# Kernel tuning notes

Measured on AMD Instinct MI355X. Metric: run time of the kernel, lower is better.

## Reference

```python
import jax, jax.numpy as jnp
import numpy as np

DIM = 384
NUM_HEADS = 12
KERNEL = 3
DILATIONS = (1, 2, 3)
B, H, W = 16, 56, 56


def _unfold(x, k, dil):
    # x: [B, c, H, W] -> [B, c, k*k, H, W]; matches nn.Unfold(k, dilation=dil,
    # padding=dil*(k-1)//2, stride=1) channel ordering [c, kh, kw].
    b, c, h, w = x.shape
    p = dil * (k - 1) // 2
    xp = jnp.pad(x, ((0, 0), (0, 0), (p, p), (p, p)))
    patches = [xp[:, :, i * dil:i * dil + h, j * dil:j * dil + w]
               for i in range(k) for j in range(k)]
    return jnp.stack(patches, axis=2)


def _dilate_attention(q, k, v, head_dim, kernel, dil):
    # q,k,v: [B, c, H, W]
    b, c, h, w = q.shape
    g = c // head_dim           # heads in this dilation branch
    kk = kernel * kernel
    scale = head_dim ** (-0.5)
    qg = q.reshape(b, g, head_dim, h * w)                       # [b,g,d,n]
    ku = _unfold(k, kernel, dil).reshape(b, g, head_dim, kk, h * w)
    vu = _unfold(v, kernel, dil).reshape(b, g, head_dim, kk, h * w)
    attn = jnp.einsum('bgdn,bgdkn->bgnk', qg, ku) * scale       # [b,g,n,kk]
    attn = jax.nn.softmax(attn, axis=-1)
    out = jnp.einsum('bgnk,bgdkn->bgnd', attn, vu)              # [b,g,n,d]
    return out.transpose(0, 2, 1, 3).reshape(b, h, w, c)        # [b,h,w,c]


def setup_inputs() -> dict:
    key = jax.random.key(0)
    kx, kq, kp = jax.random.split(key, 3)
    x = jax.random.normal(kx, (B, H, W, DIM), dtype=jnp.float32)
    w_qkv = jax.random.normal(kq, (3 * DIM, DIM), dtype=jnp.float32) * 0.02
    w_proj = jax.random.normal(kp, (DIM, DIM), dtype=jnp.float32) * 0.02
    b_proj = jnp.zeros((DIM,), dtype=jnp.float32)
    return {"x": x, "w_qkv": w_qkv, "w_proj": w_proj, "b_proj": b_proj}


def reference(x, w_qkv, w_proj, b_proj):
    b, h, w, c = x.shape
    nd = len(DILATIONS)
    cg = c // nd                # channels per dilation branch
    hd = c // NUM_HEADS         # head_dim
    xc = x.transpose(0, 3, 1, 2)                                 # [b,c,h,w]
    qkv = jnp.einsum('bchw,oc->bohw', xc, w_qkv)                 # 1x1 conv, no bias
    qkv = qkv.reshape(b, 3, nd, cg, h, w)
    outs = [_dilate_attention(qkv[:, 0, i], qkv[:, 1, i], qkv[:, 2, i],
                              hd, KERNEL, DILATIONS[i]) for i in range(nd)]
    y = jnp.stack(outs, axis=3).reshape(b, h, w, c)              # [b,h,w, nd*cg]
    return jnp.einsum('bhwc,oc->bhwo', y, w_proj) + b_proj
```

## Files before the change

### kernel.cpp

```cpp
#include <hip/hip_runtime.h>
#include <hip/hip_bf16.h>


#define NTOK 50176
#define ROWQKV 1152
#define CDIM 384

typedef _Float16 half2v __attribute__((ext_vector_type(2)));
typedef _Float16 half8 __attribute__((ext_vector_type(8)));
typedef float floatx4 __attribute__((ext_vector_type(4)));

typedef __attribute__((address_space(1))) const unsigned int GU32;
typedef __attribute__((address_space(3))) unsigned int LU32;

#define N_X4 (NTOK * CDIM / 4)
#define N_Q4 (ROWQKV * CDIM / 4)
#define N_P4 (CDIM * CDIM / 4)

__global__ __launch_bounds__(256) void conv_all(const float* __restrict__ x,
                                                const float* __restrict__ wq,
                                                const float* __restrict__ wp,
                                                _Float16* __restrict__ xh,
                                                _Float16* __restrict__ wqh,
                                                _Float16* __restrict__ wph) {
  const int total = N_X4 + N_Q4 + N_P4;
  int i = blockIdx.x * 256 + threadIdx.x;
  const int stride = gridDim.x * 256;
  for (; i < total; i += stride) {
    const float* src;
    _Float16* dst;
    int k;
    if (i < N_X4) { src = x; dst = xh; k = i; }
    else if (i < N_X4 + N_Q4) { src = wq; dst = wqh; k = i - N_X4; }
    else { src = wp; dst = wph; k = i - N_X4 - N_Q4; }
    float4 v = ((const float4*)src)[k];
    union { _Float16 h[4]; uint2 u; } o;
    o.h[0] = (_Float16)v.x; o.h[1] = (_Float16)v.y;
    o.h[2] = (_Float16)v.z; o.h[3] = (_Float16)v.w;
    ((uint2*)dst)[k] = o.u;
  }
}

template <bool HALF_OUT>
__global__ __launch_bounds__(256) void gemm3(const _Float16* __restrict__ A,
                                             const _Float16* __restrict__ B,
                                             const float* __restrict__ bias,
                                             void* __restrict__ Cout,
                                             int N, int K) {
  __shared__ _Float16 As[2][128 * 32];
  __shared__ _Float16 Bs[2][128 * 32];
  const int tid = threadIdx.x;
  const int lane = tid & 63;
  const int wv = tid >> 6;
  const int wr = wv >> 1, wc = wv & 1;

  const int nN = N >> 7;
  const int p = blockIdx.x;
  const int l = (p & 7) * (gridDim.x >> 3) + (p >> 3);
  const size_t row0 = (size_t)(l / nN) * 128;
  const int col0 = (l % nN) * 128;
  const int NT = K / 32;

  const int srow = tid >> 2;
  const int gslot = (tid & 3) ^ ((srow >> 1) & 3);
  const _Float16* Abase = A + (row0 + srow) * (size_t)K + gslot * 8;
  const _Float16* Bbase = B + ((size_t)(col0 + srow)) * (size_t)K + gslot * 8;
  char* AsB = (char*)As;
  char* BsB = (char*)Bs;

  auto stage = [&](int k0, int buf) {
    __builtin_amdgcn_global_load_lds((GU32*)(Abase + k0),
                                     (LU32*)(AsB + buf * 8192 + tid * 16), 16, 0, 0);
    __builtin_amdgcn_global_load_lds((GU32*)(Abase + (size_t)64 * K + k0),
                                     (LU32*)(AsB + buf * 8192 + tid * 16 + 4096), 16, 0, 0);
    __builtin_amdgcn_global_load_lds((GU32*)(Bbase + k0),
                                     (LU32*)(BsB + buf * 8192 + tid * 16), 16, 0, 0);
    __builtin_amdgcn_global_load_lds((GU32*)(Bbase + (size_t)64 * K + k0),
                                     (LU32*)(BsB + buf * 8192 + tid * 16 + 4096), 16, 0, 0);
  };

  const int fr = lane & 15;
  const int fq = lane >> 4;
  const int rpos = (fq ^ ((fr >> 1) & 3)) * 8;

  floatx4 acc[4][4];
#pragma unroll
  for (int i = 0; i < 4; ++i)
#pragma unroll
    for (int j = 0; j < 4; ++j) acc[i][j] = (floatx4){0.f, 0.f, 0.f, 0.f};

  stage(0, 0);
  asm volatile("s_waitcnt vmcnt(0)" ::: "memory");
  __builtin_amdgcn_s_barrier();

  int cur = 0;
  for (int t = 0; t < NT; ++t) {
    if (t + 1 < NT) {
      stage((t + 1) * 32, cur ^ 1);
      asm volatile("s_waitcnt vmcnt(4)" ::: "memory");
    } else {
      asm volatile("s_waitcnt vmcnt(0)" ::: "memory");
    }
    __builtin_amdgcn_s_barrier();
    __builtin_amdgcn_sched_barrier(0);
    half8 af[4], bf[4];
#pragma unroll
    for (int f = 0; f < 4; ++f) {
      af[f] = *(const half8*)&As[cur][(wr * 64 + f * 16 + fr) * 32 + rpos];
      bf[f] = *(const half8*)&Bs[cur][(wc * 64 + f * 16 + fr) * 32 + rpos];
    }
#pragma unroll
    for (int i = 0; i < 4; ++i)
#pragma unroll
      for (int j = 0; j < 4; ++j)
        acc[i][j] = __builtin_amdgcn_mfma_f32_16x16x32_f16(af[i], bf[j], acc[i][j], 0, 0, 0);
    __builtin_amdgcn_sched_barrier(0);
    __builtin_amdgcn_s_barrier();
    cur ^= 1;
  }

  const int crow = wr * 64 + (lane >> 4) * 4;
  const int ccol = wc * 64 + (lane & 15);
#pragma unroll
  for (int fm = 0; fm < 4; ++fm) {
#pragma unroll
    for (int fn = 0; fn < 4; ++fn) {
      const size_t r0 = (row0 + crow + fm * 16) * (size_t)N + col0 + ccol + fn * 16;
      if (HALF_OUT) {
        _Float16* C = (_Float16*)Cout;
#pragma unroll
        for (int j = 0; j < 4; ++j) C[r0 + (size_t)j * N] = (_Float16)acc[fm][fn][j];
      } else {
        float* C = (float*)Cout;
        const float bz = bias[col0 + ccol + fn * 16];
#pragma unroll
        for (int j = 0; j < 4; ++j) C[r0 + (size_t)j * N] = acc[fm][fn][j] + bz;
      }
    }
  }
}

__global__ __launch_bounds__(256) void attn_kernel(const _Float16* __restrict__ qkv,
                                                   _Float16* __restrict__ y) {
  const int idx = blockIdx.x * 256 + threadIdx.x;
  const int head = idx % 12;
  const int token = idx / 12;
  const int branch = head >> 2;
  const int dil = branch + 1;
  const int cbase = branch * 128 + (head & 3) * 32;
  const int xx = token % 56;
  const int yy = (token / 56) % 56;
  const int bimg = token / 3136;
  const float scale = 0.17677669529663687f;

  const _Float16* qp = qkv + (size_t)token * ROWQKV + cbase;
  half2v qh[16];
  *(half8*)&qh[0] = *(const half8*)(qp);
  *(half8*)&qh[4] = *(const half8*)(qp + 8);
  *(half8*)&qh[8] = *(const half8*)(qp + 16);
  *(half8*)&qh[12] = *(const half8*)(qp + 24);

  const size_t nbase = (size_t)bimg * 3136;

  float l[9];
#pragma unroll
  for (int j = 0; j < 9; ++j) {
    const int ny = yy + (j / 3 - 1) * dil;
    const int nx = xx + (j % 3 - 1) * dil;
    float d = 0.f;
    if ((unsigned)ny < 56u && (unsigned)nx < 56u) {
      const _Float16* kp = qkv + (nbase + ny * 56 + nx) * ROWQKV + 384 + cbase;
      half2v kh[16];
      *(half8*)&kh[0] = *(const half8*)(kp);
      *(half8*)&kh[4] = *(const half8*)(kp + 8);
      *(half8*)&kh[8] = *(const half8*)(kp + 16);
      *(half8*)&kh[12] = *(const half8*)(kp + 24);
#if __has_builtin(__builtin_amdgcn_fdot2)
#pragma unroll
      for (int c = 0; c < 16; ++c) d = __builtin_amdgcn_fdot2(qh[c], kh[c], d, false);
#else
#pragma unroll
      for (int c = 0; c < 16; ++c)
        d += (float)qh[c][0] * (float)kh[c][0] + (float)qh[c][1] * (float)kh[c][1];
#endif
    }
    l[j] = d * scale;
  }

  float m = l[0];
#pragma unroll
  for (int j = 1; j < 9; ++j) m = fmaxf(m, l[j]);
  float s = 0.f;
#pragma unroll
  for (int j = 0; j < 9; ++j) { l[j] = expf(l[j] - m); s += l[j]; }
  const float rs = 1.f / s;

  float out[32];
#pragma unroll
  for (int c = 0; c < 32; ++c) out[c] = 0.f;
#pragma unroll
  for (int j = 0; j < 9; ++j) {
    const int ny = yy + (j / 3 - 1) * dil;
    const int nx = xx + (j % 3 - 1) * dil;
    if ((unsigned)ny < 56u && (unsigned)nx < 56u) {
      const _Float16* vp = qkv + (nbase + ny * 56 + nx) * ROWQKV + 768 + cbase;
      half8 vh[4];
      vh[0] = *(const half8*)(vp);
      vh[1] = *(const half8*)(vp + 8);
      vh[2] = *(const half8*)(vp + 16);
      vh[3] = *(const half8*)(vp + 24);
      const float p = l[j];
#pragma unroll
      for (int g = 0; g < 4; ++g)
#pragma unroll
        for (int e = 0; e < 8; ++e) out[g * 8 + e] = fmaf(p, (float)vh[g][e], out[g * 8 + e]);
    }
  }

  _Float16* yp = y + (size_t)token * CDIM + cbase;
  half8 oh[4];
#pragma unroll
  for (int g = 0; g < 4; ++g) {
#pragma unroll
    for (int e = 0; e < 8; ++e) oh[g][e] = (_Float16)(out[g * 8 + e] * rs);
    *(half8*)(yp + g * 8) = oh[g];
  }
}

extern "C" void kernel_launch(void* const* d_in, const int* in_sizes, int n_in,
                              void* d_out, int out_size, void* d_ws, size_t ws_size,
                              hipStream_t stream) {
  const float* x = (const float*)d_in[0];
  const float* w_qkv = (const float*)d_in[1];
  const float* w_proj = (const float*)d_in[2];
  const float* b_proj = (const float*)d_in[3];
  float* out = (float*)d_out;

  _Float16* xh = (_Float16*)d_ws;
  _Float16* wqh = xh + (size_t)NTOK * CDIM;
  _Float16* wph = wqh + (size_t)ROWQKV * CDIM;
  _Float16* qkvh = wph + (size_t)CDIM * CDIM;
  _Float16* yh = qkvh + (size_t)NTOK * ROWQKV;

  conv_all<<<2048, 256, 0, stream>>>(x, w_qkv, w_proj, xh, wqh, wph);

  gemm3<true><<<(NTOK / 128) * (ROWQKV / 128), 256, 0, stream>>>(
      xh, wqh, nullptr, qkvh, ROWQKV, CDIM);

  attn_kernel<<<(NTOK * 12) / 256, 256, 0, stream>>>(qkvh, yh);

  gemm3<false><<<(NTOK / 128) * (CDIM / 128), 256, 0, stream>>>(
      yh, wph, b_proj, out, CDIM, CDIM);
}
```

Baseline: 183.3 us.

## Replace QKV GEMM with 256x256-tile 8-wave kernel and pad N to 1280

Adds a dedicated QKV projection GEMM that uses 256x256 output tiles with 512 threads, a K-tile of 64, XOR-swizzled LDS staging, split A fragment loads and s_setprio around the MFMA bursts. The output row stride is padded from 1152 to 1280 so the N dimension divides evenly into 256-wide tiles, and the attention kernel indexing and workspace layout are updated to match. The aim is more data reuse per LDS load and fewer blocks than the 128x128 generic kernel. The cost is about 11% extra MFMA work and extra qkv write traffic for padding columns that are computed from uninitialized weight rows and never read, plus lower occupancy from one large block per CU.

```diff
diff --git a/kernel.cpp b/kernel.cpp
--- a/kernel.cpp
+++ b/kernel.cpp
@@ -4,6 +4,7 @@
 
 #define NTOK 50176
 #define ROWQKV 1152
+#define NQP 1280
 #define CDIM 384
 
 typedef _Float16 half2v __attribute__((ext_vector_type(2)));
@@ -41,14 +42,125 @@
   }
 }
 
+__global__ __launch_bounds__(512, 1) void gemm_qkv8(const _Float16* __restrict__ A,
+                                                    const _Float16* __restrict__ B,
+                                                    _Float16* __restrict__ C) {
+  __shared__ _Float16 As[2][256 * 64];
+  __shared__ _Float16 Bs[2][256 * 64];
+  const int tid = threadIdx.x;
+  const int lane = tid & 63;
+  const int wv = tid >> 6;
+  const int wr = wv >> 2;
+  const int wc = wv & 3;
+  const int K = CDIM;
+
+  const int p = blockIdx.x;
+  const int xcd = p & 7, bi = p >> 3;
+  const int q = gridDim.x >> 3, r = gridDim.x & 7;
+  const int l = (xcd < r) ? xcd * (q + 1) + bi : r * (q + 1) + (xcd - r) * q + bi;
+  const int nN = NQP / 256;
+  const size_t row0 = (size_t)(l / nN) * 256;
+  const int col0 = (l % nN) * 256;
+
+  const int sr = tid >> 3;
+  const int ss = tid & 7;
+  const int aslot = (ss ^ (sr & 7)) * 8;
+  char* AsB = (char*)As;
+  char* BsB = (char*)Bs;
+
+  auto stage = [&](int kt, int buf) {
+    const int k0 = kt * 64;
+#pragma unroll
+    for (int c = 0; c < 4; ++c)
+      __builtin_amdgcn_global_load_lds(
+          (GU32*)(A + (row0 + c * 64 + sr) * (size_t)K + k0 + aslot),
+          (LU32*)(AsB + buf * 32768 + c * 8192 + tid * 16), 16, 0, 0);
+#pragma unroll
+    for (int c = 0; c < 4; ++c)
+      __builtin_amdgcn_global_load_lds(
+          (GU32*)(B + ((size_t)(col0 + c * 64 + sr)) * K + k0 + aslot),
+          (LU32*)(BsB + buf * 32768 + c * 8192 + tid * 16), 16, 0, 0);
+  };
+
+  const int fr = lane & 15;
+  const int fq = lane >> 4;
+  const int frm = fr & 7;
+
+  floatx4 acc[8][4];
+#pragma unroll
+  for (int m = 0; m < 8; ++m)
+#pragma unroll
+    for (int n = 0; n < 4; ++n) acc[m][n] = (floatx4){0.f, 0.f, 0.f, 0.f};
+
+  stage(0, 0);
+  asm volatile("s_waitcnt vmcnt(0)" ::: "memory");
+  __builtin_amdgcn_s_barrier();
+
+  for (int kt = 0; kt < 6; ++kt) {
+    const int buf = kt & 1;
+    if (kt < 5) {
+      stage(kt + 1, buf ^ 1);
+      asm volatile("s_waitcnt vmcnt(8)" ::: "memory");
+    } else {
+      asm volatile("s_waitcnt vmcnt(0)" ::: "memory");
+    }
+    __builtin_amdgcn_s_barrier();
+    __builtin_amdgcn_sched_barrier(0);
+
+    const char* ab = AsB + buf * 32768;
+    const char* bb = BsB + buf * 32768;
+    half8 af[4], bf[4];
+#pragma unroll
+    for (int kh = 0; kh < 2; ++kh) {
+      const int ko = ((((kh << 2) | fq) ^ frm) << 4);
+#pragma unroll
+      for (int half = 0; half < 2; ++half) {
+        const int mbase = half * 4;
+        if (half == 0) {
+#pragma unroll
+          for (int n = 0; n < 4; ++n)
+            bf[n] = *(const half8*)(bb + (wc * 64 + n * 16 + fr) * 128 + ko);
+        }
+#pragma unroll
+        for (int mg = 0; mg < 4; ++mg)
+          af[mg] = *(const half8*)(ab + (wr * 128 + (mbase + mg) * 16 + fr) * 128 + ko);
+        asm volatile("s_waitcnt lgkmcnt(0)" ::: "memory");
+        __builtin_amdgcn_sched_barrier(0);
+        __builtin_amdgcn_s_setprio(1);
+#pragma unroll
+        for (int mg = 0; mg < 4; ++mg)
+#pragma unroll
+          for (int n = 0; n < 4; ++n)
+            acc[mbase + mg][n] = __builtin_amdgcn_mfma_f32_16x16x32_f16(
+                af[mg], bf[n], acc[mbase + mg][n], 0, 0, 0);
+        __builtin_amdgcn_s_setprio(0);
+        __builtin_amdgcn_sched_barrier(0);
+        __builtin_amdgcn_s_barrier();
+      }
+    }
+  }
+
+  const int crow0 = wr * 128 + (lane >> 4) * 4;
+  const int ccol0 = wc * 64 + (lane & 15);
+#pragma unroll
+  for (int m = 0; m < 8; ++m) {
+#pragma unroll
+    for (int n = 0; n < 4; ++n) {
+      const size_t r0 = (row0 + crow0 + m * 16) * (size_t)NQP + col0 + ccol0 + n * 16;
+#pragma unroll
+      for (int j = 0; j < 4; ++j) C[r0 + (size_t)j * NQP] = (_Float16)acc[m][n][j];
+    }
+  }
+}
+
 template <bool HALF_OUT>
 __global__ __launch_bounds__(256) void gemm3(const _Float16* __restrict__ A,
                                              const _Float16* __restrict__ B,
                                              const float* __restrict__ bias,
                                              void* __restrict__ Cout,
                                              int N, int K) {
-  __shared__ _Float16 As[2][128 * 32];
-  __shared__ _Float16 Bs[2][128 * 32];
+  __shared__ _Float16 Asl[2][128 * 32];
+  __shared__ _Float16 Bsl[2][128 * 32];
   const int tid = threadIdx.x;
   const int lane = tid & 63;
   const int wv = tid >> 6;
@@ -65,8 +177,8 @@
   const int gslot = (tid & 3) ^ ((srow >> 1) & 3);
   const _Float16* Abase = A + (row0 + srow) * (size_t)K + gslot * 8;
   const _Float16* Bbase = B + ((size_t)(col0 + srow)) * (size_t)K + gslot * 8;
-  char* AsB = (char*)As;
-  char* BsB = (char*)Bs;
+  char* AsB = (char*)Asl;
+  char* BsB = (char*)Bsl;
 
   auto stage = [&](int k0, int buf) {
     __builtin_amdgcn_global_load_lds((GU32*)(Abase + k0),
@@ -106,8 +218,8 @@
     half8 af[4], bf[4];
 #pragma unroll
     for (int f = 0; f < 4; ++f) {
-      af[f] = *(const half8*)&As[cur][(wr * 64 + f * 16 + fr) * 32 + rpos];
-      bf[f] = *(const half8*)&Bs[cur][(wc * 64 + f * 16 + fr) * 32 + rpos];
+      af[f] = *(const half8*)&Asl[cur][(wr * 64 + f * 16 + fr) * 32 + rpos];
+      bf[f] = *(const half8*)&Bsl[cur][(wc * 64 + f * 16 + fr) * 32 + rpos];
     }
 #pragma unroll
     for (int i = 0; i < 4; ++i)
@@ -127,14 +239,14 @@
     for (int fn = 0; fn < 4; ++fn) {
       const size_t r0 = (row0 + crow + fm * 16) * (size_t)N + col0 + ccol + fn * 16;
       if (HALF_OUT) {
-        _Float16* C = (_Float16*)Cout;
-#pragma unroll
-        for (int j = 0; j < 4; ++j) C[r0 + (size_t)j * N] = (_Float16)acc[fm][fn][j];
+        _Float16* Cc = (_Float16*)Cout;
+#pragma unroll
+        for (int j = 0; j < 4; ++j) Cc[r0 + (size_t)j * N] = (_Float16)acc[fm][fn][j];
       } else {
-        float* C = (float*)Cout;
+        float* Cc = (float*)Cout;
         const float bz = bias[col0 + ccol + fn * 16];
 #pragma unroll
-        for (int j = 0; j < 4; ++j) C[r0 + (size_t)j * N] = acc[fm][fn][j] + bz;
+        for (int j = 0; j < 4; ++j) Cc[r0 + (size_t)j * N] = acc[fm][fn][j] + bz;
       }
     }
   }
@@ -153,7 +265,7 @@
   const int bimg = token / 3136;
   const float scale = 0.17677669529663687f;
 
-  const _Float16* qp = qkv + (size_t)token * ROWQKV + cbase;
+  const _Float16* qp = qkv + (size_t)token * NQP + cbase;
   half2v qh[16];
   *(half8*)&qh[0] = *(const half8*)(qp);
   *(half8*)&qh[4] = *(const half8*)(qp + 8);
@@ -169,7 +281,7 @@
     const int nx = xx + (j % 3 - 1) * dil;
     float d = 0.f;
     if ((unsigned)ny < 56u && (unsigned)nx < 56u) {
-      const _Float16* kp = qkv + (nbase + ny * 56 + nx) * ROWQKV + 384 + cbase;
+      const _Float16* kp = qkv + (nbase + ny * 56 + nx) * NQP + 384 + cbase;
       half2v kh[16];
       *(half8*)&kh[0] = *(const half8*)(kp);
       *(half8*)&kh[4] = *(const half8*)(kp + 8);
@@ -203,7 +315,7 @@
     const int ny = yy + (j / 3 - 1) * dil;
     const int nx = xx + (j % 3 - 1) * dil;
     if ((unsigned)ny < 56u && (unsigned)nx < 56u) {
-      const _Float16* vp = qkv + (nbase + ny * 56 + nx) * ROWQKV + 768 + cbase;
+      const _Float16* vp = qkv + (nbase + ny * 56 + nx) * NQP + 768 + cbase;
       half8 vh[4];
       vh[0] = *(const half8*)(vp);
       vh[1] = *(const half8*)(vp + 8);
@@ -238,14 +350,13 @@
 
   _Float16* xh = (_Float16*)d_ws;
   _Float16* wqh = xh + (size_t)NTOK * CDIM;
-  _Float16* wph = wqh + (size_t)ROWQKV * CDIM;
+  _Float16* wph = wqh + (size_t)NQP * CDIM;
   _Float16* qkvh = wph + (size_t)CDIM * CDIM;
-  _Float16* yh = qkvh + (size_t)NTOK * ROWQKV;
+  _Float16* yh = qkvh + (size_t)NTOK * NQP;
 
   conv_all<<<2048, 256, 0, stream>>>(x, w_qkv, w_proj, xh, wqh, wph);
 
-  gemm3<true><<<(NTOK / 128) * (ROWQKV / 128), 256, 0, stream>>>(
-      xh, wqh, nullptr, qkvh, ROWQKV, CDIM);
+  gemm_qkv8<<<(NTOK / 256) * (NQP / 256), 512, 0, stream>>>(xh, wqh, qkvh);
 
   attn_kernel<<<(NTOK * 12) / 256, 256, 0, stream>>>(qkvh, yh);
 
```

New measurement: 187.2 us. 2.1% more time.

## Tile dilated attention per 8x8 patch with shared-memory K/V halo staging

Applied to the files above, without the earlier changes.

Replaces the per-thread attention kernel, which gathered nine K and V rows straight from global memory, with a templated kernel per dilation. Each kernel loads an 8x8 token tile plus its dilation halo of K/V into padded shared memory, then serves every neighbour lookup from LDS. Out-of-image neighbours are stored as zeros, so the bounds branches in the inner loops go away. The cost is three separate launches and a large LDS footprint for the biggest dilation (about 110KB), which limits occupancy to roughly one block per CU. Some GEMM variables are also renamed.

```diff
diff --git a/kernel.cpp b/kernel.cpp
--- a/kernel.cpp
+++ b/kernel.cpp
@@ -47,8 +47,8 @@
                                              const float* __restrict__ bias,
                                              void* __restrict__ Cout,
                                              int N, int K) {
-  __shared__ _Float16 As[2][128 * 32];
-  __shared__ _Float16 Bs[2][128 * 32];
+  __shared__ _Float16 Asl[2][128 * 32];
+  __shared__ _Float16 Bsl[2][128 * 32];
   const int tid = threadIdx.x;
   const int lane = tid & 63;
   const int wv = tid >> 6;
@@ -65,8 +65,8 @@
   const int gslot = (tid & 3) ^ ((srow >> 1) & 3);
   const _Float16* Abase = A + (row0 + srow) * (size_t)K + gslot * 8;
   const _Float16* Bbase = B + ((size_t)(col0 + srow)) * (size_t)K + gslot * 8;
-  char* AsB = (char*)As;
-  char* BsB = (char*)Bs;
+  char* AsB = (char*)Asl;
+  char* BsB = (char*)Bsl;
 
   auto stage = [&](int k0, int buf) {
     __builtin_amdgcn_global_load_lds((GU32*)(Abase + k0),
@@ -106,8 +106,8 @@
     half8 af[4], bf[4];
 #pragma unroll
     for (int f = 0; f < 4; ++f) {
-      af[f] = *(const half8*)&As[cur][(wr * 64 + f * 16 + fr) * 32 + rpos];
-      bf[f] = *(const half8*)&Bs[cur][(wc * 64 + f * 16 + fr) * 32 + rpos];
+      af[f] = *(const half8*)&Asl[cur][(wr * 64 + f * 16 + fr) * 32 + rpos];
+      bf[f] = *(const half8*)&Bsl[cur][(wc * 64 + f * 16 + fr) * 32 + rpos];
     }
 #pragma unroll
     for (int i = 0; i < 4; ++i)
@@ -127,63 +127,85 @@
     for (int fn = 0; fn < 4; ++fn) {
       const size_t r0 = (row0 + crow + fm * 16) * (size_t)N + col0 + ccol + fn * 16;
       if (HALF_OUT) {
-        _Float16* C = (_Float16*)Cout;
-#pragma unroll
-        for (int j = 0; j < 4; ++j) C[r0 + (size_t)j * N] = (_Float16)acc[fm][fn][j];
+        _Float16* Cc = (_Float16*)Cout;
+#pragma unroll
+        for (int j = 0; j < 4; ++j) Cc[r0 + (size_t)j * N] = (_Float16)acc[fm][fn][j];
       } else {
-        float* C = (float*)Cout;
+        float* Cc = (float*)Cout;
         const float bz = bias[col0 + ccol + fn * 16];
 #pragma unroll
-        for (int j = 0; j < 4; ++j) C[r0 + (size_t)j * N] = acc[fm][fn][j] + bz;
+        for (int j = 0; j < 4; ++j) Cc[r0 + (size_t)j * N] = acc[fm][fn][j] + bz;
       }
     }
   }
 }
 
-__global__ __launch_bounds__(256) void attn_kernel(const _Float16* __restrict__ qkv,
-                                                   _Float16* __restrict__ y) {
-  const int idx = blockIdx.x * 256 + threadIdx.x;
-  const int head = idx % 12;
-  const int token = idx / 12;
-  const int branch = head >> 2;
-  const int dil = branch + 1;
-  const int cbase = branch * 128 + (head & 3) * 32;
-  const int xx = token % 56;
-  const int yy = (token / 56) % 56;
-  const int bimg = token / 3136;
+template <int DIL>
+__global__ __launch_bounds__(256) void attn_tile(const _Float16* __restrict__ qkv,
+                                                 _Float16* __restrict__ y) {
+  constexpr int H = 8 + 2 * DIL;
+  constexpr int NROW = H * H;
+  __shared__ char kv[NROW * 560];
+  const int tid = threadIdx.x;
+  const int head = tid & 3;
+  const int tok = tid >> 2;
+  const int ly = tok >> 3, lx = tok & 7;
+  const int branch = DIL - 1;
+  const int cb = branch * 128;
+  const int bimg = blockIdx.y;
+  const int ty0 = (blockIdx.x / 7) * 8;
+  const int tx0 = (blockIdx.x % 7) * 8;
+  const size_t base = (size_t)bimg * 3136;
   const float scale = 0.17677669529663687f;
 
-  const _Float16* qp = qkv + (size_t)token * ROWQKV + cbase;
+  constexpr int NG = NROW * 32;
+  for (int g = tid; g < NG; g += 256) {
+    const int r = g >> 5, sl = g & 31;
+    const int gy = ty0 - DIL + r / H;
+    const int gx = tx0 - DIL + r % H;
+    uint4 val = make_uint4(0u, 0u, 0u, 0u);
+    if ((unsigned)gy < 56u && (unsigned)gx < 56u) {
+      const int off = (sl < 16) ? (384 + cb + sl * 8) : (768 + cb + (sl - 16) * 8);
+      val = *(const uint4*)(qkv + (base + gy * 56 + gx) * ROWQKV + off);
+    }
+    *(uint4*)(kv + r * 560 + sl * 16) = val;
+  }
+
+  const int gty = ty0 + ly, gtx = tx0 + lx;
+  const _Float16* qp = qkv + (base + gty * 56 + gtx) * ROWQKV + cb + head * 32;
   half2v qh[16];
   *(half8*)&qh[0] = *(const half8*)(qp);
   *(half8*)&qh[4] = *(const half8*)(qp + 8);
   *(half8*)&qh[8] = *(const half8*)(qp + 16);
   *(half8*)&qh[12] = *(const half8*)(qp + 24);
 
-  const size_t nbase = (size_t)bimg * 3136;
+  __syncthreads();
+
+  int rtap[9];
+#pragma unroll
+  for (int j = 0; j < 9; ++j) {
+    const int dy = j / 3 - 1, dx = j % 3 - 1;
+    rtap[j] = (ly + DIL + dy * DIL) * H + (lx + DIL + dx * DIL);
+  }
 
   float l[9];
 #pragma unroll
   for (int j = 0; j < 9; ++j) {
-    const int ny = yy + (j / 3 - 1) * dil;
-    const int nx = xx + (j % 3 - 1) * dil;
+    const char* kp = kv + rtap[j] * 560 + head * 64;
+    half2v kh[16];
+    *(half8*)&kh[0] = *(const half8*)(kp);
+    *(half8*)&kh[4] = *(const half8*)(kp + 16);
+    *(half8*)&kh[8] = *(const half8*)(kp + 32);
+    *(half8*)&kh[12] = *(const half8*)(kp + 48);
     float d = 0.f;
-    if ((unsigned)ny < 56u && (unsigned)nx < 56u) {
-      const _Float16* kp = qkv + (nbase + ny * 56 + nx) * ROWQKV + 384 + cbase;
-      half2v kh[16];
-      *(half8*)&kh[0] = *(const half8*)(kp);
-      *(half8*)&kh[4] = *(const half8*)(kp + 8);
-      *(half8*)&kh[8] = *(const half8*)(kp + 16);
-      *(half8*)&kh[12] = *(const half8*)(kp + 24);
 #if __has_builtin(__builtin_amdgcn_fdot2)
 #pragma unroll
-      for (int c = 0; c < 16; ++c) d = __builtin_amdgcn_fdot2(qh[c], kh[c], d, false);
+    for (int c = 0; c < 16; ++c) d = __builtin_amdgcn_fdot2(qh[c], kh[c], d, false);
 #else
 #pragma unroll
-      for (int c = 0; c < 16; ++c)
-        d += (float)qh[c][0] * (float)kh[c][0] + (float)qh[c][1] * (float)kh[c][1];
+    for (int c = 0; c < 16; ++c)
+      d += (float)qh[c][0] * (float)kh[c][0] + (float)qh[c][1] * (float)kh[c][1];
 #endif
-    }
     l[j] = d * scale;
   }
 
@@ -200,24 +222,20 @@
   for (int c = 0; c < 32; ++c) out[c] = 0.f;
 #pragma unroll
   for (int j = 0; j < 9; ++j) {
-    const int ny = yy + (j / 3 - 1) * dil;
-    const int nx = xx + (j % 3 - 1) * dil;
-    if ((unsigned)ny < 56u && (unsigned)nx < 56u) {
-      const _Float16* vp = qkv + (nbase + ny * 56 + nx) * ROWQKV + 768 + cbase;
-      half8 vh[4];
-      vh[0] = *(const half8*)(vp);
-      vh[1] = *(const half8*)(vp + 8);
-      vh[2] = *(const half8*)(vp + 16);
-      vh[3] = *(const half8*)(vp + 24);
-      const float p = l[j];
-#pragma unroll
-      for (int g = 0; g < 4; ++g)
-#pragma unroll
-        for (int e = 0; e < 8; ++e) out[g * 8 + e] = fmaf(p, (float)vh[g][e], out[g * 8 + e]);
-    }
-  }
-
-  _Float16* yp = y + (size_t)token * CDIM + cbase;
+    const char* vp = kv + rtap[j] * 560 + 256 + head * 64;
+    half8 vh[4];
+    vh[0] = *(const half8*)(vp);
+    vh[1] = *(const half8*)(vp + 16);
+    vh[2] = *(const half8*)(vp + 32);
+    vh[3] = *(const half8*)(vp + 48);
+    const float p = l[j];
+#pragma unroll
+    for (int g = 0; g < 4; ++g)
+#pragma unroll
+      for (int e = 0; e < 8; ++e) out[g * 8 + e] = fmaf(p, (float)vh[g][e], out[g * 8 + e]);
+  }
+
+  _Float16* yp = y + (base + gty * 56 + gtx) * (size_t)CDIM + cb + head * 32;
   half8 oh[4];
 #pragma unroll
   for (int g = 0; g < 4; ++g) {
@@ -247,7 +265,9 @@
   gemm3<true><<<(NTOK / 128) * (ROWQKV / 128), 256, 0, stream>>>(
       xh, wqh, nullptr, qkvh, ROWQKV, CDIM);
 
-  attn_kernel<<<(NTOK * 12) / 256, 256, 0, stream>>>(qkvh, yh);
+  attn_tile<1><<<dim3(49, 16), 256, 0, stream>>>(qkvh, yh);
+  attn_tile<2><<<dim3(49, 16), 256, 0, stream>>>(qkvh, yh);
+  attn_tile<3><<<dim3(49, 16), 256, 0, stream>>>(qkvh, yh);
 
   gemm3<false><<<(NTOK / 128) * (CDIM / 128), 256, 0, stream>>>(
       yh, wph, b_proj, out, CDIM, CDIM);
```

Measured after the change: 214.4 us. 17.0% more time.
